# Optimization experiments

Hardware: AMD Instinct MI355X
Metric: run time of the kernel (lower is better)

## Reference

```python
import jax, jax.numpy as jnp
import numpy as np

N_NODES = 25000
N_EDGES = 400000
N_GRAPHS = 1000
HID = 185
IN_CH = 9
EPS = 1e-5  # BatchNorm eps (eval mode: uses running stats)


def setup_inputs() -> dict:
    key = jax.random.key(0)
    ks = jax.random.split(key, 12)
    x = jax.random.normal(ks[0], (N_NODES, IN_CH), jnp.float32)
    edge_index = jax.random.randint(ks[1], (2, N_EDGES), 0, N_NODES, jnp.int32)
    batch = jnp.sort(jax.random.randint(ks[2], (N_NODES,), 0, N_GRAPHS, jnp.int32))
    W0 = jax.random.normal(ks[3], (IN_CH, HID), jnp.float32) * 0.3
    b0 = jnp.zeros((HID,), jnp.float32)
    W_h = jax.random.normal(ks[4], (3, HID, HID), jnp.float32) * 0.07
    b_h = jnp.zeros((3, HID), jnp.float32)
    bn_gamma = 1.0 + 0.1 * jax.random.normal(ks[5], (4, HID), jnp.float32)
    bn_beta = 0.1 * jax.random.normal(ks[6], (4, HID), jnp.float32)
    bn_mean = 0.1 * jax.random.normal(ks[7], (4, HID), jnp.float32)
    bn_var = jax.random.uniform(ks[8], (4, HID), jnp.float32, 0.5, 1.5)
    W_jk = jax.random.normal(ks[9], (4 * HID, HID), jnp.float32) * 0.05
    b_jk = jnp.zeros((HID,), jnp.float32)
    W_out = jax.random.normal(ks[10], (HID, 1), jnp.float32) * 0.1
    b_out = jnp.zeros((1,), jnp.float32)
    return dict(x=x, edge_index=edge_index, batch=batch, W0=W0, b0=b0,
                W_h=W_h, b_h=b_h, bn_gamma=bn_gamma, bn_beta=bn_beta,
                bn_mean=bn_mean, bn_var=bn_var, W_jk=W_jk, b_jk=b_jk,
                W_out=W_out, b_out=b_out)


def reference(x, edge_index, batch, W0, b0, W_h, b_h, bn_gamma, bn_beta,
              bn_mean, bn_var, W_jk, b_jk, W_out, b_out):
    N = x.shape[0]
    # GCN normalization with self-loops (gcn_norm, edge_weight = 1)
    loop = jnp.arange(N, dtype=edge_index.dtype)
    src = jnp.concatenate([edge_index[0], loop])  # [E+N]
    dst = jnp.concatenate([edge_index[1], loop])  # [E+N]
    deg = jax.ops.segment_sum(jnp.ones_like(dst, dtype=x.dtype), dst, num_segments=N)
    dis = jnp.where(deg > 0, jax.lax.rsqrt(jnp.maximum(deg, 1.0)), 0.0)
    enorm = dis[src] * dis[dst]  # [E+N]

    def gcn_conv(h, W, b):
        h = h @ W                                   # [N, HID]
        msg = h[src] * enorm[:, None]               # gather + scale, [E+N, HID]
        return jax.ops.segment_sum(msg, dst, num_segments=N) + b

    def bn_relu(h, i):
        h = (h - bn_mean[i]) * jax.lax.rsqrt(bn_var[i] + EPS) * bn_gamma[i] + bn_beta[i]
        return jax.nn.relu(h)  # dropout is identity in eval mode

    xs = []
    h = bn_relu(gcn_conv(x, W0, b0), 0)
    xs.append(h)
    for i in range(3):
        h = bn_relu(gcn_conv(h, W_h[i], b_h[i]), i + 1)
        xs.append(h)
    # JumpingKnowledge 'cat' + internal lin (740 -> 185)
    h = jnp.concatenate(xs, axis=-1) @ W_jk + b_jk  # [N, HID]
    # global_max_pool over graphs
    pooled = jax.ops.segment_max(h, batch, num_segments=N_GRAPHS)  # [G, HID]
    return pooled @ W_out + b_out  # [G, 1]
```

## Files before the change

### kernel.cpp

```cpp
#include <hip/hip_runtime.h>
#include <hip/hip_bf16.h>

#define N_NODES 25000
#define N_EDGES 400000
#define N_GRAPHS 1000
#define HID 185
#define EPS 1e-5f
#define XPITCH 768
#define APITCH 56

typedef __attribute__((ext_vector_type(8))) short bf16x8;
typedef __attribute__((ext_vector_type(4))) float f32x4;

__device__ __forceinline__ short f2bf(float f) {
    union { float f; unsigned u; } v; v.f = f;
    unsigned r = v.u + 0x7FFFu + ((v.u >> 16) & 1u);
    return (short)(r >> 16);
}
__device__ __forceinline__ float bfl(unsigned u) { return __uint_as_float(u << 16); }
__device__ __forceinline__ float bfh(unsigned u) { return __uint_as_float(u & 0xFFFF0000u); }
__device__ __forceinline__ unsigned pk2(float lo, float hi) {
    return (unsigned)(unsigned short)f2bf(lo) | ((unsigned)(unsigned short)f2bf(hi) << 16);
}

__global__ void k_init(int* cnt, int* cursor, unsigned* pooled) {
    int i = blockIdx.x * blockDim.x + threadIdx.x;
    if (i < N_NODES) { cnt[i] = 0; cursor[i] = 0; }
    if (i < N_GRAPHS * HID) pooled[i] = 0u;
}

__global__ void k_deg(const int* __restrict__ dst, int* cnt, int E) {
    int i = blockIdx.x * blockDim.x + threadIdx.x;
    if (i < E) atomicAdd(&cnt[dst[i]], 1);
}

__global__ void k_dis(const int* __restrict__ cnt, float* dis, int N) {
    int i = blockIdx.x * blockDim.x + threadIdx.x;
    if (i < N) dis[i] = rsqrtf((float)(cnt[i] + 1));
}

__global__ __launch_bounds__(256) void k_scan_part(const int* __restrict__ cnt,
                                                   int* __restrict__ bsum, int N) {
    int i = blockIdx.x * 256 + threadIdx.x;
    int v = (i < N) ? cnt[i] : 0;
    #pragma unroll
    for (int off = 32; off; off >>= 1) v += __shfl_down(v, off);
    __shared__ int s[4];
    if ((threadIdx.x & 63) == 0) s[threadIdx.x >> 6] = v;
    __syncthreads();
    if (threadIdx.x == 0) bsum[blockIdx.x] = s[0] + s[1] + s[2] + s[3];
}

__global__ __launch_bounds__(128) void k_scan_mid(const int* __restrict__ bsum,
                                                  int* __restrict__ boff, int NB) {
    __shared__ int s[128];
    int t = threadIdx.x;
    int v = (t < NB) ? bsum[t] : 0;
    s[t] = v; __syncthreads();
    for (int off = 1; off < 128; off <<= 1) {
        int x = (t >= off) ? s[t - off] : 0;
        __syncthreads();
        s[t] += x;
        __syncthreads();
    }
    if (t < NB) boff[t] = s[t] - v;
}

__global__ __launch_bounds__(256) void k_scan_add(const int* __restrict__ cnt,
                                                  const int* __restrict__ boff,
                                                  int* __restrict__ rowptr, int N) {
    __shared__ int s[256];
    int t = threadIdx.x;
    int i = blockIdx.x * 256 + t;
    int v = (i < N) ? cnt[i] : 0;
    s[t] = v; __syncthreads();
    for (int off = 1; off < 256; off <<= 1) {
        int x = (t >= off) ? s[t - off] : 0;
        __syncthreads();
        s[t] += x;
        __syncthreads();
    }
    if (i < N) rowptr[i + 1] = boff[blockIdx.x] + s[t];
    if (i == 0) rowptr[0] = 0;
}

__global__ void k_scatter(const int* __restrict__ src, const int* __restrict__ dst,
                          const float* __restrict__ dis, const int* __restrict__ rowptr,
                          int* cursor, int* __restrict__ csr_src,
                          float* __restrict__ csr_w, int E) {
    int e = blockIdx.x * blockDim.x + threadIdx.x;
    if (e < E) {
        int d = dst[e];
        int s = src[e];
        int pos = atomicAdd(&cursor[d], 1);
        int o = rowptr[d] + pos;
        csr_src[o] = s;
        csr_w[o] = dis[s];
    }
}

__global__ void k_prep_w(const float* __restrict__ W_h, const float* __restrict__ W_jk,
                         const float* __restrict__ b0, const float* __restrict__ b_h,
                         const float* __restrict__ gamma, const float* __restrict__ beta,
                         const float* __restrict__ mean, const float* __restrict__ var,
                         short* __restrict__ Wt_h, short* __restrict__ Wt_jk,
                         float* __restrict__ bnsc, float* __restrict__ bnsh) {
    int idx = blockIdx.x * 256 + threadIdx.x;
    const int HW = 3 * 192 * 192;
    const int JW = 192 * 768;
    if (idx < HW) {
        int l = idx / (192 * 192);
        int r = idx % (192 * 192);
        int n = r / 192, k = r % 192;
        float v = (n < HID && k < HID) ? W_h[(l * HID + k) * HID + n] : 0.0f;
        Wt_h[idx] = f2bf(v);
    } else if (idx < HW + JW) {
        int j2 = idx - HW;
        int n = j2 / 768, kk = j2 % 768;
        int l = kk / 192, j = kk % 192;
        float v = (n < HID && j < HID) ? W_jk[(l * HID + j) * HID + n] : 0.0f;
        Wt_jk[j2] = f2bf(v);
    } else if (idx < HW + JW + 4 * 192) {
        int li = idx - HW - JW;
        int l = li / 192, c = li % 192;
        float sc = 0.0f, sh = 0.0f;
        if (c < HID) {
            float bb = (l == 0) ? b0[c] : b_h[(l - 1) * HID + c];
            sc = rsqrtf(var[l * HID + c] + EPS) * gamma[l * HID + c];
            sh = (bb - mean[l * HID + c]) * sc + beta[l * HID + c];
        }
        bnsc[li] = sc;
        bnsh[li] = sh;
    }
}

__global__ void k_aggr0(const float* __restrict__ x, const float* __restrict__ dis,
                        const int* __restrict__ rowptr, const int* __restrict__ csr_src,
                        const float* __restrict__ csr_w, float* __restrict__ xa, int N) {
    int idx = blockIdx.x * blockDim.x + threadIdx.x;
    int n = idx >> 4;
    int c = idx & 15;
    if (n >= N || c >= 9) return;
    float dn = dis[n];
    float acc = x[n * 9 + c] * dn;
    int e = rowptr[n], end = rowptr[n + 1];
    for (; e + 4 <= end; e += 4) {
        int s0 = csr_src[e], s1 = csr_src[e + 1], s2 = csr_src[e + 2], s3 = csr_src[e + 3];
        float w0 = csr_w[e], w1 = csr_w[e + 1], w2 = csr_w[e + 2], w3 = csr_w[e + 3];
        float v0 = x[s0 * 9 + c], v1 = x[s1 * 9 + c], v2 = x[s2 * 9 + c], v3 = x[s3 * 9 + c];
        acc += v0 * w0 + v1 * w1 + v2 * w2 + v3 * w3;
    }
    for (; e < end; ++e)
        acc += x[csr_src[e] * 9 + c] * csr_w[e];
    xa[n * 9 + c] = acc * dn;
}

__global__ __launch_bounds__(192) void k_gemm0(const float* __restrict__ A,
                                               const float* __restrict__ W,
                                               const float* __restrict__ bnsc,
                                               const float* __restrict__ bnsh,
                                               short* __restrict__ xcat, int N) {
    __shared__ float As[8 * 9];
    const int tid = threadIdx.x;
    const int r0 = blockIdx.x * 8;
    for (int idx = tid; idx < 72; idx += 192) {
        int r = idx & 7, k = idx >> 3;
        int row = r0 + r;
        As[idx] = (row < N) ? A[row * 9 + k] : 0.0f;
    }
    __syncthreads();
    const int c = tid;
    float res[8];
    #pragma unroll
    for (int r = 0; r < 8; ++r) res[r] = 0.0f;
    if (c < HID) {
        float acc[8] = {0,0,0,0,0,0,0,0};
        for (int k = 0; k < 9; ++k) {
            float w = W[k * HID + c];
            #pragma unroll
            for (int r = 0; r < 8; ++r) acc[r] += As[k * 8 + r] * w;
        }
        float sc = bnsc[c], sh = bnsh[c];
        #pragma unroll
        for (int r = 0; r < 8; ++r)
            res[r] = fmaxf(acc[r] * sc + sh, 0.0f);
    }
    #pragma unroll
    for (int r = 0; r < 8; ++r) {
        int row = r0 + r;
        if (row < N) xcat[row * XPITCH + c] = (c < HID) ? f2bf(res[r]) : (short)0;
    }
}

template<int KCH, bool POOL>
__global__ __launch_bounds__(256) void k_mgemm(const short* __restrict__ A,
                                               const short* __restrict__ Bt,
                                               const float* __restrict__ bias,
                                               short* __restrict__ Cout,
                                               const int* __restrict__ batch,
                                               unsigned* __restrict__ pooled, int N) {
    __shared__ short As[64 * APITCH];
    __shared__ short Bs[192 * APITCH];
    __shared__ int sb[64];
    const int tid = threadIdx.x;
    const int wave = tid >> 6;
    const int lane = tid & 63;
    const int quad = lane >> 4;
    const int lm = lane & 15;
    const int r0 = blockIdx.x * 64;
    const int KTOT = KCH * 32;
    const int arow = tid >> 2, aseg = tid & 3;

    if (POOL) {
        if (tid < 64) sb[tid] = (r0 + tid < N) ? batch[r0 + tid] : 0;
    }

    f32x4 acc[4][3];
    #pragma unroll
    for (int i = 0; i < 4; ++i)
        #pragma unroll
        for (int j = 0; j < 3; ++j) acc[i][j] = (f32x4){0.f, 0.f, 0.f, 0.f};

    for (int kc = 0; kc < KCH; ++kc) {
        const int k0 = kc * 32;
        {
            int grow = r0 + arow;
            bf16x8 v = (bf16x8){0,0,0,0,0,0,0,0};
            if (grow < N) v = *(const bf16x8*)(A + grow * XPITCH + k0 + aseg * 8);
            *(bf16x8*)(As + arow * APITCH + aseg * 8) = v;
        }
        #pragma unroll
        for (int i = 0; i < 3; ++i) {
            int u = tid + i * 256;
            int n = u >> 2, seg = u & 3;
            bf16x8 v = *(const bf16x8*)(Bt + n * KTOT + k0 + seg * 8);
            *(bf16x8*)(Bs + n * APITCH + seg * 8) = v;
        }
        __syncthreads();
        bf16x8 a[4], b[3];
        #pragma unroll
        for (int mt = 0; mt < 4; ++mt)
            a[mt] = *(const bf16x8*)(As + (mt * 16 + lm) * APITCH + quad * 8);
        #pragma unroll
        for (int nt = 0; nt < 3; ++nt)
            b[nt] = *(const bf16x8*)(Bs + (wave * 48 + nt * 16 + lm) * APITCH + quad * 8);
        #pragma unroll
        for (int mt = 0; mt < 4; ++mt)
            #pragma unroll
            for (int nt = 0; nt < 3; ++nt)
                acc[mt][nt] = __builtin_amdgcn_mfma_f32_16x16x32_bf16(a[mt], b[nt], acc[mt][nt], 0, 0, 0);
        __syncthreads();
    }
    #pragma unroll
    for (int mt = 0; mt < 4; ++mt) {
        #pragma unroll
        for (int nt = 0; nt < 3; ++nt) {
            int col = wave * 48 + nt * 16 + lm;
            if (POOL) {
                if (col < HID) {
                    float bb = bias[col];
                    #pragma unroll
                    for (int r = 0; r < 4; ++r) {
                        int lrow = mt * 16 + quad * 4 + r;
                        if (r0 + lrow < N) {
                            float v = acc[mt][nt][r] + bb;
                            unsigned b32 = __float_as_uint(v);
                            unsigned enc = (b32 & 0x80000000u) ? ~b32 : (b32 | 0x80000000u);
                            atomicMax(&pooled[sb[lrow] * HID + col], enc);
                        }
                    }
                }
            } else {
                #pragma unroll
                for (int r = 0; r < 4; ++r) {
                    int row = r0 + mt * 16 + quad * 4 + r;
                    if (row < N) Cout[row * 192 + col] = f2bf(acc[mt][nt][r]);
                }
            }
        }
    }
}

__global__ __launch_bounds__(256) void k_aggr_bn(const short* __restrict__ tmp16,
                                                 const float* __restrict__ dis,
                                                 const int* __restrict__ rowptr,
                                                 const int* __restrict__ csr_src,
                                                 const float* __restrict__ csr_w,
                                                 const float* __restrict__ bnsc,
                                                 const float* __restrict__ bnsh,
                                                 short* __restrict__ outp, int N) {
    int n = (blockIdx.x << 2) + (threadIdx.x >> 6);
    if (n >= N) return;
    int lane = threadIdx.x & 63;
    int c0 = (lane < 48) ? (lane << 2) : 0;
    float dn = dis[n];
    float a0, a1, a2, a3;
    {
        uint2 v = *(const uint2*)(tmp16 + (size_t)n * 192 + c0);
        a0 = bfl(v.x) * dn; a1 = bfh(v.x) * dn; a2 = bfl(v.y) * dn; a3 = bfh(v.y) * dn;
    }
    int e = rowptr[n], end = rowptr[n + 1];
    for (; e + 4 <= end; e += 4) {
        int s0 = csr_src[e], s1 = csr_src[e + 1], s2 = csr_src[e + 2], s3 = csr_src[e + 3];
        float w0 = csr_w[e], w1 = csr_w[e + 1], w2 = csr_w[e + 2], w3 = csr_w[e + 3];
        uint2 v0 = *(const uint2*)(tmp16 + (size_t)s0 * 192 + c0);
        uint2 v1 = *(const uint2*)(tmp16 + (size_t)s1 * 192 + c0);
        uint2 v2 = *(const uint2*)(tmp16 + (size_t)s2 * 192 + c0);
        uint2 v3 = *(const uint2*)(tmp16 + (size_t)s3 * 192 + c0);
        a0 += bfl(v0.x) * w0; a1 += bfh(v0.x) * w0; a2 += bfl(v0.y) * w0; a3 += bfh(v0.y) * w0;
        a0 += bfl(v1.x) * w1; a1 += bfh(v1.x) * w1; a2 += bfl(v1.y) * w1; a3 += bfh(v1.y) * w1;
        a0 += bfl(v2.x) * w2; a1 += bfh(v2.x) * w2; a2 += bfl(v2.y) * w2; a3 += bfh(v2.y) * w2;
        a0 += bfl(v3.x) * w3; a1 += bfh(v3.x) * w3; a2 += bfl(v3.y) * w3; a3 += bfh(v3.y) * w3;
    }
    for (; e < end; ++e) {
        int s = csr_src[e];
        float w = csr_w[e];
        uint2 v = *(const uint2*)(tmp16 + (size_t)s * 192 + c0);
        a0 += bfl(v.x) * w; a1 += bfh(v.x) * w; a2 += bfl(v.y) * w; a3 += bfh(v.y) * w;
    }
    float4 sc = *(const float4*)(bnsc + c0);
    float4 sh = *(const float4*)(bnsh + c0);
    float o0 = fmaxf(a0 * dn * sc.x + sh.x, 0.0f);
    float o1 = fmaxf(a1 * dn * sc.y + sh.y, 0.0f);
    float o2 = fmaxf(a2 * dn * sc.z + sh.z, 0.0f);
    float o3 = fmaxf(a3 * dn * sc.w + sh.w, 0.0f);
    if (lane < 48) {
        uint2 p;
        p.x = pk2(o0, o1);
        p.y = pk2(o2, o3);
        *(uint2*)(outp + (size_t)n * XPITCH + c0) = p;
    }
}

__global__ __launch_bounds__(64) void k_out(const unsigned* __restrict__ pooled,
                                            const float* __restrict__ W_out,
                                            const float* __restrict__ b_out,
                                            float* __restrict__ out, int G) {
    int g = blockIdx.x;
    int lane = threadIdx.x;
    float sum = 0.0f;
    for (int c = lane; c < HID; c += 64) {
        unsigned u = pooled[g * HID + c];
        unsigned bits = (u & 0x80000000u) ? (u & 0x7FFFFFFFu) : ~u;
        sum += __uint_as_float(bits) * W_out[c];
    }
    #pragma unroll
    for (int off = 32; off; off >>= 1) sum += __shfl_down(sum, off);
    if (lane == 0) out[g] = sum + b_out[0];
}

extern "C" void kernel_launch(void* const* d_in, const int* in_sizes, int n_in,
                              void* d_out, int out_size, void* d_ws, size_t ws_size,
                              hipStream_t stream) {
    const float* x      = (const float*)d_in[0];
    const int*   ei     = (const int*)  d_in[1];
    const int*   batch  = (const int*)  d_in[2];
    const float* W0     = (const float*)d_in[3];
    const float* b0     = (const float*)d_in[4];
    const float* W_h    = (const float*)d_in[5];
    const float* b_h    = (const float*)d_in[6];
    const float* gamma  = (const float*)d_in[7];
    const float* beta   = (const float*)d_in[8];
    const float* mean   = (const float*)d_in[9];
    const float* var    = (const float*)d_in[10];
    const float* W_jk   = (const float*)d_in[11];
    const float* b_jk   = (const float*)d_in[12];
    const float* W_out  = (const float*)d_in[13];
    const float* b_out  = (const float*)d_in[14];
    float* out = (float*)d_out;

    const int N = N_NODES, E = N_EDGES, G = N_GRAPHS, H = HID;
    const int NB = (N + 255) / 256;

    float* dis   = (float*)d_ws;
    float* xa    = dis + 25024;
    float* csr_w = xa + 225024;
    float* bnsc  = csr_w + 400000;
    float* bnsh  = bnsc + 768;
    short* xcat  = (short*)(bnsh + 768);
    short* tmp16 = xcat + 19200000;
    short* Wt_h  = tmp16 + 4800000;
    short* Wt_jk = Wt_h + 110592;
    int* rowptr  = (int*)(Wt_jk + 147456);
    int* cnt     = rowptr + 25024;
    int* cursor  = cnt + 25024;
    int* csr_src = cursor + 25024;
    int* bsum    = csr_src + 400000;
    int* boff    = bsum + 128;
    unsigned* pooled = (unsigned*)(boff + 128);

    const int* src = ei;
    const int* dst = ei + E;

    k_init<<<(G * H + 255) / 256, 256, 0, stream>>>(cnt, cursor, pooled);
    k_deg<<<(E + 255) / 256, 256, 0, stream>>>(dst, cnt, E);
    k_dis<<<(N + 255) / 256, 256, 0, stream>>>(cnt, dis, N);
    k_scan_part<<<NB, 256, 0, stream>>>(cnt, bsum, N);
    k_scan_mid<<<1, 128, 0, stream>>>(bsum, boff, NB);
    k_scan_add<<<NB, 256, 0, stream>>>(cnt, boff, rowptr, N);
    k_scatter<<<(E + 255) / 256, 256, 0, stream>>>(src, dst, dis, rowptr, cursor,
                                                   csr_src, csr_w, E);
    k_prep_w<<<(3 * 192 * 192 + 192 * 768 + 4 * 192 + 255) / 256, 256, 0, stream>>>(
        W_h, W_jk, b0, b_h, gamma, beta, mean, var, Wt_h, Wt_jk, bnsc, bnsh);

    k_aggr0<<<(N * 16 + 255) / 256, 256, 0, stream>>>(x, dis, rowptr, csr_src, csr_w, xa, N);
    k_gemm0<<<(N + 7) / 8, 192, 0, stream>>>(xa, W0, bnsc, bnsh, xcat, N);

    const int MB = (N + 63) / 64;
    for (int l = 1; l < 4; ++l) {
        k_mgemm<6, false><<<MB, 256, 0, stream>>>(xcat + (l - 1) * 192,
                                                  Wt_h + (l - 1) * 192 * 192,
                                                  nullptr, tmp16, nullptr, nullptr, N);
        k_aggr_bn<<<(N + 3) / 4, 256, 0, stream>>>(tmp16, dis, rowptr, csr_src, csr_w,
                                                   bnsc + l * 192, bnsh + l * 192,
                                                   xcat + l * 192, N);
    }

    k_mgemm<24, true><<<MB, 256, 0, stream>>>(xcat, Wt_jk, b_jk, nullptr, batch, pooled, N);

    k_out<<<G, 64, 0, stream>>>(pooled, W_out, b_out, out, G);
}
```

Baseline: 349.8 us.

## Replace atomic max pooling with fp32 JK output and segmented pool kernel

The final JK GEMM now writes its fp32 result to a workspace buffer instead of doing a per-element atomicMax into an encoded pooled array. A new kernel binary-searches the sorted batch array for each graph's node range, takes the column max, and fuses the bias add and output dot product. This removes heavy atomic contention and the pooled-buffer init, at the cost of writing and re-reading an N x 192 fp32 array. The LDS pitch for the GEMM tiles is also cut from 56 to 36, which changes bank-conflict behaviour and LDS footprint.

```diff
diff --git a/kernel.cpp b/kernel.cpp
--- a/kernel.cpp
+++ b/kernel.cpp
@@ -7,7 +7,7 @@
 #define HID 185
 #define EPS 1e-5f
 #define XPITCH 768
-#define APITCH 56
+#define APITCH 36
 
 typedef __attribute__((ext_vector_type(8))) short bf16x8;
 typedef __attribute__((ext_vector_type(4))) float f32x4;
@@ -23,10 +23,9 @@
     return (unsigned)(unsigned short)f2bf(lo) | ((unsigned)(unsigned short)f2bf(hi) << 16);
 }
 
-__global__ void k_init(int* cnt, int* cursor, unsigned* pooled) {
+__global__ void k_init(int* cnt, int* cursor) {
     int i = blockIdx.x * blockDim.x + threadIdx.x;
     if (i < N_NODES) { cnt[i] = 0; cursor[i] = 0; }
-    if (i < N_GRAPHS * HID) pooled[i] = 0u;
 }
 
 __global__ void k_deg(const int* __restrict__ dst, int* cnt, int E) {
@@ -192,16 +191,12 @@
     }
 }
 
-template<int KCH, bool POOL>
+template<int KCH, bool F32OUT>
 __global__ __launch_bounds__(256) void k_mgemm(const short* __restrict__ A,
                                                const short* __restrict__ Bt,
-                                               const float* __restrict__ bias,
-                                               short* __restrict__ Cout,
-                                               const int* __restrict__ batch,
-                                               unsigned* __restrict__ pooled, int N) {
+                                               void* __restrict__ Cout, int N) {
     __shared__ short As[64 * APITCH];
     __shared__ short Bs[192 * APITCH];
-    __shared__ int sb[64];
     const int tid = threadIdx.x;
     const int wave = tid >> 6;
     const int lane = tid & 63;
@@ -211,10 +206,6 @@
     const int KTOT = KCH * 32;
     const int arow = tid >> 2, aseg = tid & 3;
 
-    if (POOL) {
-        if (tid < 64) sb[tid] = (r0 + tid < N) ? batch[r0 + tid] : 0;
-    }
-
     f32x4 acc[4][3];
     #pragma unroll
     for (int i = 0; i < 4; ++i)
@@ -256,25 +247,12 @@
         #pragma unroll
         for (int nt = 0; nt < 3; ++nt) {
             int col = wave * 48 + nt * 16 + lm;
-            if (POOL) {
-                if (col < HID) {
-                    float bb = bias[col];
-                    #pragma unroll
-                    for (int r = 0; r < 4; ++r) {
-                        int lrow = mt * 16 + quad * 4 + r;
-                        if (r0 + lrow < N) {
-                            float v = acc[mt][nt][r] + bb;
-                            unsigned b32 = __float_as_uint(v);
-                            unsigned enc = (b32 & 0x80000000u) ? ~b32 : (b32 | 0x80000000u);
-                            atomicMax(&pooled[sb[lrow] * HID + col], enc);
-                        }
-                    }
-                }
-            } else {
-                #pragma unroll
-                for (int r = 0; r < 4; ++r) {
-                    int row = r0 + mt * 16 + quad * 4 + r;
-                    if (row < N) Cout[row * 192 + col] = f2bf(acc[mt][nt][r]);
+            #pragma unroll
+            for (int r = 0; r < 4; ++r) {
+                int row = r0 + mt * 16 + quad * 4 + r;
+                if (row < N) {
+                    if (F32OUT) ((float*)Cout)[row * 192 + col] = acc[mt][nt][r];
+                    else        ((short*)Cout)[row * 192 + col] = f2bf(acc[mt][nt][r]);
                 }
             }
         }
@@ -332,21 +310,36 @@
     }
 }
 
-__global__ __launch_bounds__(64) void k_out(const unsigned* __restrict__ pooled,
-                                            const float* __restrict__ W_out,
-                                            const float* __restrict__ b_out,
-                                            float* __restrict__ out, int G) {
-    int g = blockIdx.x;
-    int lane = threadIdx.x;
-    float sum = 0.0f;
-    for (int c = lane; c < HID; c += 64) {
-        unsigned u = pooled[g * HID + c];
-        unsigned bits = (u & 0x80000000u) ? (u & 0x7FFFFFFFu) : ~u;
-        sum += __uint_as_float(bits) * W_out[c];
-    }
-    #pragma unroll
-    for (int off = 32; off; off >>= 1) sum += __shfl_down(sum, off);
-    if (lane == 0) out[g] = sum + b_out[0];
+__global__ __launch_bounds__(192) void k_pool_out(const float* __restrict__ tmpf,
+                                                  const int* __restrict__ batch,
+                                                  const float* __restrict__ b_jk,
+                                                  const float* __restrict__ W_out,
+                                                  const float* __restrict__ b_out,
+                                                  float* __restrict__ out, int N) {
+    __shared__ int bounds[2];
+    __shared__ float partial[3];
+    const int g = blockIdx.x;
+    const int tid = threadIdx.x;
+    if (tid < 2) {
+        int key = g + tid;
+        int lo = 0, hi = N;
+        while (lo < hi) {
+            int mid = (lo + hi) >> 1;
+            if (batch[mid] < key) lo = mid + 1; else hi = mid;
+        }
+        bounds[tid] = lo;
+    }
+    __syncthreads();
+    const int beg = bounds[0], end = bounds[1];
+    float mx = -3.4e38f;
+    for (int n = beg; n < end; ++n)
+        mx = fmaxf(mx, tmpf[(size_t)n * 192 + tid]);
+    float p = (tid < HID) ? (mx + b_jk[tid]) * W_out[tid] : 0.0f;
+    #pragma unroll
+    for (int off = 32; off; off >>= 1) p += __shfl_down(p, off);
+    if ((tid & 63) == 0) partial[tid >> 6] = p;
+    __syncthreads();
+    if (tid == 0) out[g] = partial[0] + partial[1] + partial[2] + b_out[0];
 }
 
 extern "C" void kernel_launch(void* const* d_in, const int* in_sizes, int n_in,
@@ -377,7 +370,8 @@
     float* csr_w = xa + 225024;
     float* bnsc  = csr_w + 400000;
     float* bnsh  = bnsc + 768;
-    short* xcat  = (short*)(bnsh + 768);
+    float* tmpf  = bnsh + 768;
+    short* xcat  = (short*)(tmpf + 4800000);
     short* tmp16 = xcat + 19200000;
     short* Wt_h  = tmp16 + 4800000;
     short* Wt_jk = Wt_h + 110592;
@@ -387,14 +381,13 @@
     int* csr_src = cursor + 25024;
     int* bsum    = csr_src + 400000;
     int* boff    = bsum + 128;
-    unsigned* pooled = (unsigned*)(boff + 128);
 
     const int* src = ei;
     const int* dst = ei + E;
 
-    k_init<<<(G * H + 255) / 256, 256, 0, stream>>>(cnt, cursor, pooled);
+    k_init<<<NB, 256, 0, stream>>>(cnt, cursor);
     k_deg<<<(E + 255) / 256, 256, 0, stream>>>(dst, cnt, E);
-    k_dis<<<(N + 255) / 256, 256, 0, stream>>>(cnt, dis, N);
+    k_dis<<<NB, 256, 0, stream>>>(cnt, dis, N);
     k_scan_part<<<NB, 256, 0, stream>>>(cnt, bsum, N);
     k_scan_mid<<<1, 128, 0, stream>>>(bsum, boff, NB);
     k_scan_add<<<NB, 256, 0, stream>>>(cnt, boff, rowptr, N);
@@ -409,14 +402,13 @@
     const int MB = (N + 63) / 64;
     for (int l = 1; l < 4; ++l) {
         k_mgemm<6, false><<<MB, 256, 0, stream>>>(xcat + (l - 1) * 192,
-                                                  Wt_h + (l - 1) * 192 * 192,
-                                                  nullptr, tmp16, nullptr, nullptr, N);
+                                                  Wt_h + (l - 1) * 192 * 192, tmp16, N);
         k_aggr_bn<<<(N + 3) / 4, 256, 0, stream>>>(tmp16, dis, rowptr, csr_src, csr_w,
                                                    bnsc + l * 192, bnsh + l * 192,
                                                    xcat + l * 192, N);
     }
 
-    k_mgemm<24, true><<<MB, 256, 0, stream>>>(xcat, Wt_jk, b_jk, nullptr, batch, pooled, N);
-
-    k_out<<<G, 64, 0, stream>>>(pooled, W_out, b_out, out, G);
-}
+    k_mgemm<24, true><<<MB, 256, 0, stream>>>(xcat, Wt_jk, tmpf, N);
+
+    k_pool_out<<<G, 192, 0, stream>>>(tmpf, batch, b_jk, W_out, b_out, out, N);
+}
```

Measured after the change: 315.8 us. 1.11x faster.
